# Performance work log

Measured on AMD Instinct MI355X. Metric: run time of the kernel, lower is better.

Reference implementation:

```python
import jax, jax.numpy as jnp
import numpy as np
import math

EMSIZE = 512
NX = 2048        # emsize * (layer_id+1), layer_id=3
H = NX // EMSIZE # 4 heads of size EMSIZE (grow_head path)
B, S = 4, 2048
EPS = 1e-5


def _layernorm(x, g, b):
    u = jnp.mean(x, axis=-1, keepdims=True)
    s = jnp.mean((x - u) ** 2, axis=-1, keepdims=True)
    return g * (x - u) / jnp.sqrt(s + EPS) + b


def _gelu(x):
    # OpenAI tanh-approx gelu, exactly as in source
    return 0.5 * x * (1.0 + jnp.tanh(jnp.sqrt(2.0 / jnp.pi) * (x + 0.044715 * x ** 3)))


def setup_inputs() -> dict:
    key = jax.random.key(0)
    ks = jax.random.split(key, 8)
    std = 0.02
    return {
        "x": jax.random.normal(ks[0], (B, S, NX), jnp.float32),
        "w_qkv": jax.random.normal(ks[1], (NX, 3 * NX), jnp.float32) * std,
        "b_qkv": jnp.zeros((3 * NX,), jnp.float32),
        "w_ao": jax.random.normal(ks[2], (NX, NX), jnp.float32) * std,
        "b_ao": jnp.zeros((NX,), jnp.float32),
        "ln1_g": jnp.ones((NX,), jnp.float32),
        "ln1_b": jnp.zeros((NX,), jnp.float32),
        "w_fc": jax.random.normal(ks[3], (NX, 4 * NX), jnp.float32) * std,
        "b_fc": jnp.zeros((4 * NX,), jnp.float32),
        "w_pr": jax.random.normal(ks[4], (4 * NX, NX), jnp.float32) * std,
        "b_pr": jnp.zeros((NX,), jnp.float32),
        "ln2_g": jnp.ones((NX,), jnp.float32),
        "ln2_b": jnp.zeros((NX,), jnp.float32),
        "w_out": jax.random.normal(ks[5], (NX, EMSIZE), jnp.float32) * std,
        "b_out": jnp.zeros((EMSIZE,), jnp.float32),
    }


def reference(x, w_qkv, b_qkv, w_ao, b_ao, ln1_g, ln1_b, w_fc, b_fc,
              w_pr, b_pr, ln2_g, ln2_b, w_out, b_out):
    Bx, Sx, _ = x.shape
    # --- multi-head attention ---
    qkv = x @ w_qkv + b_qkv                       # [B,S,3*NX]
    q, k, v = jnp.split(qkv, 3, axis=-1)
    q = q.reshape(Bx, Sx, H, EMSIZE).transpose(0, 2, 1, 3)  # [B,H,S,E]
    k = k.reshape(Bx, Sx, H, EMSIZE).transpose(0, 2, 1, 3)
    v = v.reshape(Bx, Sx, H, EMSIZE).transpose(0, 2, 1, 3)
    w = jnp.einsum("bhqe,bhke->bhqk", q, k) / jnp.sqrt(jnp.float32(EMSIZE))
    alen = jnp.arange(Sx)
    mask = alen[None, :] <= alen[:, None]          # causal [S,S]
    # source: w*mask + -1e9*(1-mask) == where(mask, w, -1e9)
    w = jnp.where(mask[None, None], w, jnp.float32(-1e9))
    w = jax.nn.softmax(w, axis=-1)
    a = jnp.einsum("bhqk,bhke->bhqe", w, v)        # [B,H,S,E]
    a = a.transpose(0, 2, 1, 3).reshape(Bx, Sx, NX)
    a = a @ w_ao + b_ao
    # --- residual + LN + MLP + LN ---
    n = _layernorm(x + a, ln1_g, ln1_b)
    m = (_gelu(n @ w_fc + b_fc)) @ w_pr + b_pr
    h = _layernorm(n + m, ln2_g, ln2_b)
    # --- final projection + grow_head concat ---
    h = h @ w_out + b_out                          # [B,S,EMSIZE]
    h = h.reshape(Bx, Sx, 1, EMSIZE)
    j = x.reshape(Bx, Sx, H, EMSIZE)
    out = jnp.concatenate([j, h], axis=-2)         # [B,S,H+1,E]
    return out.reshape(Bx, Sx, (H + 1) * EMSIZE)
```

## Files before the change

### kernel.cpp

```cpp
#include <hip/hip_runtime.h>
#include <hip/hip_bf16.h>
#include <math.h>

using bf16 = __hip_bfloat16;
typedef __attribute__((ext_vector_type(8))) short s16x8;
typedef __attribute__((ext_vector_type(4))) float f32x4;

struct __align__(16) B8 { bf16 v[8]; };
struct __align__(8)  B4 { bf16 v[4]; };

__device__ __forceinline__ float b2f(bf16 x){ return __bfloat162float(x); }
__device__ __forceinline__ bf16  f2b(float x){ return __float2bfloat16(x); }

enum { EPI_QKV=0, EPI_AO=3, EPI_FC=4, EPI_PR=5, EPI_OUT=6 };

#define SCHED0 __builtin_amdgcn_sched_barrier(0)
#define PRIO1  __builtin_amdgcn_s_setprio(1)
#define PRIO0  __builtin_amdgcn_s_setprio(0)
#define BAR    __builtin_amdgcn_s_barrier()
#define VM8    asm volatile("s_waitcnt vmcnt(8)" ::: "memory")
#define VM4    asm volatile("s_waitcnt vmcnt(4)" ::: "memory")
#define VM2    asm volatile("s_waitcnt vmcnt(2)" ::: "memory")
#define VM0    asm volatile("s_waitcnt vmcnt(0)" ::: "memory")
#define LGKM0  asm volatile("s_waitcnt lgkmcnt(0)" ::: "memory")
#define AS1    const __attribute__((address_space(1))) void*
#define AS3    __attribute__((address_space(3))) void*

template<int EPI>
__launch_bounds__(512, 2)
__global__ void gemm256(const bf16* __restrict__ A, const bf16* __restrict__ B,
                        void* __restrict__ Cv, const float* __restrict__ bias,
                        const void* __restrict__ res,
                        int K, int lda, int ldb, int ldc, int ldres, int nbx)
{
    extern __shared__ __align__(16) bf16 lds[];
    bf16* Asl = lds;
    bf16* Bsl = lds + 32768;

    const int nwg = (int)gridDim.x;
    int wg = (int)blockIdx.x;
    if ((nwg & 7) == 0) wg = (wg & 7)*(nwg >> 3) + (wg >> 3);
    const int bx = wg % nbx, by = wg / nbx;
    const long m0 = (long)by*256, n0 = (long)bx*256;

    const int tid = threadIdx.x, wave = tid>>6, lane = tid&63;
    const int wr = wave>>2, wc = wave&3;
    const int NT = K>>6;

    const int fr = lane&15;
    const int fc = (lane>>4) ^ ((fr>>1)&3);
    const bf16* aRd = Asl + (wr*128 + fr)*32 + fc*8;
    const bf16* bRd = Bsl + (wc*64  + fr)*32 + fc*8;

    #define LDA4(dst, slot, mq) { \
        dst[0] = *(const s16x8*)(aRd + (slot)*8192 + (mq)*2048);        \
        dst[1] = *(const s16x8*)(aRd + (slot)*8192 + (mq)*2048 + 512);  \
        dst[2] = *(const s16x8*)(aRd + (slot)*8192 + (mq)*2048 + 1024); \
        dst[3] = *(const s16x8*)(aRd + (slot)*8192 + (mq)*2048 + 1536); }
    #define LDB4(dst, slot) { \
        dst[0] = *(const s16x8*)(bRd + (slot)*8192);        \
        dst[1] = *(const s16x8*)(bRd + (slot)*8192 + 512);  \
        dst[2] = *(const s16x8*)(bRd + (slot)*8192 + 1024); \
        dst[3] = *(const s16x8*)(bRd + (slot)*8192 + 1536); }

    const int grow = tid>>2;
    const int gch  = (tid&3) ^ ((grow>>1)&3);
    const bf16* aP0 = A + (m0 + grow)*(long)lda + gch*8;
    const bf16* aP1 = aP0 + 128*(long)lda;
    const bf16* bP0 = B + (n0 + grow)*(long)ldb + gch*8;
    const bf16* bP1 = bP0 + 128*(long)ldb;
    bf16* aWr = Asl + wave*512;
    bf16* bWr = Bsl + wave*512;

    #define STGA(slot, koff) { \
        __builtin_amdgcn_global_load_lds((AS1)(aP0 + (koff)), (AS3)(aWr + (slot)*8192), 16, 0, 0); \
        __builtin_amdgcn_global_load_lds((AS1)(aP1 + (koff)), (AS3)(aWr + (slot)*8192 + 4096), 16, 0, 0); }
    #define STGB(slot, koff) { \
        __builtin_amdgcn_global_load_lds((AS1)(bP0 + (koff)), (AS3)(bWr + (slot)*8192), 16, 0, 0); \
        __builtin_amdgcn_global_load_lds((AS1)(bP1 + (koff)), (AS3)(bWr + (slot)*8192 + 4096), 16, 0, 0); }

    f32x4 acc[8][4];
    #pragma unroll
    for (int i=0;i<8;++i)
        #pragma unroll
        for (int j=0;j<4;++j)
            #pragma unroll
            for (int r=0;r<4;++r) acc[i][j][r] = 0.f;

    auto CL = [&](int mq, const s16x8* af, const s16x8* bf){
        #pragma unroll
        for (int ii=0; ii<4; ++ii)
            #pragma unroll
            for (int j=0; j<4; ++j)
                acc[mq*4+ii][j] = __builtin_amdgcn_mfma_f32_16x16x32_bf16(af[ii], bf[j], acc[mq*4+ii][j], 0,0,0);
    };

    s16x8 af0[4], af1[4], bf0[4], bf1[4];

    STGA(0,0);  STGB(0,0);
    STGA(1,32); STGB(1,32);
    STGA(2,64); STGB(2,64);
    VM8; SCHED0; BAR;
    LDB4(bf0, 0); LDA4(af0, 0, 0);
    STGA(3,96);
    SCHED0; BAR;

    for (int TT=0; TT<=NT-4; TT+=2){
        PRIO1; CL(0,af0,bf0); PRIO0;
        LDA4(af1, 0, 1);
        STGB(3, 96);
        VM8; SCHED0; BAR;
        PRIO1; CL(1,af1,bf0); PRIO0;
        LDB4(bf1, 1); LDA4(af0, 1, 0);
        STGA(0, 128);
        SCHED0; BAR;
        PRIO1; CL(0,af0,bf1); PRIO0;
        LDA4(af1, 1, 1);
        STGB(0, 128);
        VM8; SCHED0; BAR;
        PRIO1; CL(1,af1,bf1); PRIO0;
        LDB4(bf0, 2); LDA4(af0, 2, 0);
        STGA(1, 160);
        SCHED0; BAR;
        PRIO1; CL(0,af0,bf0); PRIO0;
        LDA4(af1, 2, 1);
        STGB(1, 160);
        VM8; SCHED0; BAR;
        PRIO1; CL(1,af1,bf0); PRIO0;
        LDB4(bf1, 3); LDA4(af0, 3, 0);
        STGA(2, 192);
        SCHED0; BAR;
        PRIO1; CL(0,af0,bf1); PRIO0;
        LDA4(af1, 3, 1);
        STGB(2, 192);
        VM8; SCHED0; BAR;
        PRIO1; CL(1,af1,bf1); PRIO0;
        LDB4(bf0, 0); LDA4(af0, 0, 0);
        STGA(3, 224);
        SCHED0; BAR;
        aP0 += 128; aP1 += 128; bP0 += 128; bP1 += 128;
    }

    PRIO1; CL(0,af0,bf0); PRIO0;
    LDA4(af1, 0, 1);
    STGB(3, 96);
    VM8; SCHED0; BAR;
    PRIO1; CL(1,af1,bf0); PRIO0;
    LDB4(bf1, 1); LDA4(af0, 1, 0);
    SCHED0; BAR;
    PRIO1; CL(0,af0,bf1); PRIO0;
    LDA4(af1, 1, 1);
    VM4; SCHED0; BAR;
    PRIO1; CL(1,af1,bf1); PRIO0;
    LDB4(bf0, 2); LDA4(af0, 2, 0);
    SCHED0; BAR;
    PRIO1; CL(0,af0,bf0); PRIO0;
    LDA4(af1, 2, 1);
    VM0; SCHED0; BAR;
    PRIO1; CL(1,af1,bf0); PRIO0;
    LDB4(bf1, 3); LDA4(af0, 3, 0);
    SCHED0; BAR;
    PRIO1; CL(0,af0,bf1); PRIO0;
    LDA4(af1, 3, 1);
    PRIO1; CL(1,af1,bf1); PRIO0;

    #undef STGA
    #undef STGB
    #undef LDA4
    #undef LDB4

    const int colB = lane&15;
    const int row4 = (lane>>4)*4;
    #pragma unroll
    for (int i=0;i<8;++i){
        #pragma unroll
        for (int j=0;j<4;++j){
            const long mmb = m0 + wr*128 + i*16 + row4;
            const long nn  = n0 + wc*64  + j*16 + colB;
            #pragma unroll
            for (int r=0;r<4;++r){
                const long mm = mmb + r;
                const float v = acc[i][j][r];
                if constexpr (EPI==EPI_AO){
                    ((float*)Cv)[mm*ldc + nn] = v + bias[nn] + ((const float*)res)[mm*ldres + nn];
                } else if constexpr (EPI==EPI_PR){
                    ((float*)Cv)[mm*ldc + nn] = v + bias[nn] + b2f(((const bf16*)res)[mm*ldres + nn]);
                } else if constexpr (EPI==EPI_FC){
                    const float tt = v + bias[nn];
                    const float g = 0.5f*tt*(1.f + tanhf(0.7978845608028654f*(tt + 0.044715f*tt*tt*tt)));
                    ((bf16*)Cv)[mm*ldc + nn] = f2b(g);
                } else if constexpr (EPI==EPI_OUT){
                    ((float*)Cv)[mm*ldc + nn] = v + bias[nn];
                } else {
                    ((bf16*)Cv)[mm*ldc + nn] = f2b(v + bias[nn]);
                }
            }
        }
    }
}

__launch_bounds__(512, 2)
__global__ void fattn(const bf16* __restrict__ qkv, const bf16* __restrict__ vt,
                      bf16* __restrict__ outp)
{
    extern __shared__ __align__(16) bf16 sh[];
    bf16* sQ = sh;
    bf16* sK = sh + 32768;
    bf16* sP = sh + 57344;
    bf16* sV = sh + 65536;
    float* part = (float*)(sh + 32768);

    const int bid = blockIdx.x;
    const int xcd = bid&7, t5 = bid>>3, rnd = t5>>5, ci = t5&31;
    const int bh = xcd*2 + rnd, b = bh>>2, h = bh&3;
    const int ib = 31 - ci;
    const int njb = (ib>>1) + 1;
    const int tid = threadIdx.x, wave = tid>>6, lane = tid&63;
    const int wr = wave>>2, wc = wave&3;
    const int fr = lane&15, fg = lane>>4;

    const bf16* Qg = qkv + ((long)b*2048 + ib*64)*6144 + h*512;
    const bf16* Kg = qkv + (long)b*2048*6144 + 2048 + h*512;
    const bf16* Vtb = vt + (long)bh*1048576;
    const float SCALE = 0.044194173824159216f;

    #define STGQ { _Pragma("unroll") for (int l=0;l<8;++l){                          \
        const int row = l*8 + (tid>>6);                                              \
        const int c   = (tid&63) ^ (row&7);                                          \
        __builtin_amdgcn_global_load_lds((AS1)(Qg + (long)row*6144 + c*8),           \
            (AS3)(sQ + l*4096 + wave*512 + lane*8), 16,0,0); } }
    #define STGK(slot, ec, KJ) { _Pragma("unroll") for (int l=0;l<2;++l){            \
        const int row = l*64 + (tid>>3);                                             \
        const int c   = (tid&7) ^ (row&7);                                           \
        __builtin_amdgcn_global_load_lds((AS1)((KJ) + (long)row*6144 + (ec)*64 + c*8),\
            (AS3)(sK + (slot)*8192 + l*4096 + wave*512 + lane*8), 16,0,0); } }
    #define STGV(buf, kf, eh, VJ) { _Pragma("unroll") for (int l=0;l<2;++l){         \
        const int row = l*128 + (tid>>2);                                            \
        const int c   = (tid&3) ^ ((row + (row>>2))&3);                              \
        __builtin_amdgcn_global_load_lds((AS1)((VJ) + (long)((eh)*256+row)*2048 + (kf)*32 + c*8),\
            (AS3)(sV + (buf)*8192 + l*4096 + wave*512 + lane*8), 16,0,0); } }

    f32x4 acc[2][8];
    #pragma unroll
    for (int m=0;m<2;++m)
        #pragma unroll
        for (int j=0;j<8;++j)
            #pragma unroll
            for (int r=0;r<4;++r) acc[m][j][r] = 0.f;
    float l_l[2][4];
    #pragma unroll
    for (int m=0;m<2;++m){ l_l[m][0]=0.f; l_l[m][1]=0.f; l_l[m][2]=0.f; l_l[m][3]=0.f; }

    const bf16* KgJ = Kg;
    const bf16* VtJ = Vtb;

    STGQ;
    STGK(0, 0, KgJ);
    STGK(1, 1, KgJ);
    VM2; SCHED0; BAR;

    for (int jb=0; jb<njb; ++jb){
        const bool last = (jb == njb-1);
        f32x4 sacc[2][2];
        #pragma unroll
        for (int m=0;m<2;++m)
            #pragma unroll
            for (int nf=0;nf<2;++nf)
                #pragma unroll
                for (int r=0;r<4;++r) sacc[m][nf][r] = 0.f;

        #pragma unroll
        for (int ec=0; ec<8; ++ec){
            const int slot = ec%3;
            s16x8 qa[2][2], kb[2][2];
            #pragma unroll
            for (int m=0;m<2;++m)
                #pragma unroll
                for (int kk=0;kk<2;++kk){
                    const int row = wr*32 + m*16 + fr;
                    const int c = (ec*2+kk)*4 + fg;
                    qa[m][kk] = *(const s16x8*)(sQ + row*512 + ((c ^ (row&7))*8));
                }
            #pragma unroll
            for (int nf=0;nf<2;++nf)
                #pragma unroll
                for (int kk=0;kk<2;++kk){
                    const int row = wc*32 + nf*16 + fr;
                    const int c = kk*4 + fg;
                    kb[nf][kk] = *(const s16x8*)(sK + slot*8192 + row*64 + ((c ^ (row&7))*8));
                }
            if (ec < 6) STGK((ec+2)%3, ec+2, KgJ);
            PRIO1;
            #pragma unroll
            for (int m=0;m<2;++m)
                #pragma unroll
                for (int nf=0;nf<2;++nf)
                    #pragma unroll
                    for (int kk=0;kk<2;++kk)
                        sacc[m][nf] = __builtin_amdgcn_mfma_f32_16x16x32_bf16(qa[m][kk], kb[nf][kk], sacc[m][nf], 0,0,0);
            PRIO0;
            if (ec < 6) { VM2; } else if (ec == 6) { VM0; }
            SCHED0; BAR;
        }

        const int doff = (njb-1)*128 - ib*64;
        #pragma unroll
        for (int m=0;m<2;++m)
            #pragma unroll
            for (int nf=0;nf<2;++nf)
                #pragma unroll
                for (int r=0;r<4;++r){
                    float pv = __expf(sacc[m][nf][r]*SCALE - 4.0f);
                    const int rl = wr*32 + m*16 + fg*4 + r;
                    const int cl = wc*32 + nf*16 + fr;
                    if (last && (cl + doff > rl)) pv = 0.f;
                    sP[rl*128 + (((cl>>3) ^ (rl&15))*8) + (cl&7)] = f2b(pv);
                    l_l[m][r] += pv;
                }
        STGV(0, 0, 0, VtJ);
        if (!last){ STGK(0, 0, KgJ + 786432); STGK(1, 1, KgJ + 786432); }
        if (!last){ VM4; } else { VM0; }
        LGKM0; SCHED0; BAR;

        s16x8 pa[2];
        #pragma unroll
        for (int v=0; v<8; ++v){
            const int kf = v>>1, eh = v&1, buf = v&1;
            if (eh == 0){
                #pragma unroll
                for (int m=0;m<2;++m){
                    const int row = wr*32 + m*16 + fr;
                    const int c = kf*4 + fg;
                    pa[m] = *(const s16x8*)(sP + row*128 + ((c ^ (row&15))*8));
                }
            }
            s16x8 vb[4];
            #pragma unroll
            for (int nf=0;nf<4;++nf){
                const int row = wc*64 + nf*16 + fr;
                vb[nf] = *(const s16x8*)(sV + buf*8192 + row*32 + (((fg ^ ((row + (row>>2))&3)))*8));
            }
            if (v < 7) STGV((v+1)&1, (v+1)>>1, (v+1)&1, VtJ);
            PRIO1;
            #pragma unroll
            for (int m=0;m<2;++m)
                #pragma unroll
                for (int nf=0;nf<4;++nf)
                    acc[m][eh*4+nf] = __builtin_amdgcn_mfma_f32_16x16x32_bf16(pa[m], vb[nf], acc[m][eh*4+nf], 0,0,0);
            PRIO0;
            if (v < 7) { VM0; }
            SCHED0; BAR;
        }
        KgJ += 786432;
        VtJ += 128;
    }

    #pragma unroll
    for (int m=0;m<2;++m)
        #pragma unroll
        for (int r=0;r<4;++r){
            float v = l_l[m][r];
            v += __shfl_xor(v, 1); v += __shfl_xor(v, 2);
            v += __shfl_xor(v, 4); v += __shfl_xor(v, 8);
            l_l[m][r] = v;
        }
    if (fr == 0){
        #pragma unroll
        for (int m=0;m<2;++m)
            #pragma unroll
            for (int r=0;r<4;++r)
                part[(wr*32 + m*16 + fg*4 + r)*4 + wc] = l_l[m][r];
    }
    LGKM0; SCHED0; BAR;

    bf16* orow = outp + ((long)b*2048 + ib*64)*2048 + h*512;
    #pragma unroll
    for (int m=0;m<2;++m)
        #pragma unroll
        for (int r=0;r<4;++r){
            const int rl = wr*32 + m*16 + fg*4 + r;
            const f32x4 pp = *(const f32x4*)(part + rl*4);
            const float rinv = 1.f/(pp[0]+pp[1]+pp[2]+pp[3]);
            #pragma unroll
            for (int j=0;j<8;++j){
                const int e = (j>>2)*256 + wc*64 + (j&3)*16 + fr;
                orow[(long)rl*2048 + e] = f2b(acc[m][j][r]*rinv);
            }
        }
    #undef STGQ
    #undef STGK
    #undef STGV
}

__launch_bounds__(256)
__global__ void wtrans(const float* __restrict__ W, bf16* __restrict__ Wt, int Kd, int Nd){
    __shared__ float t[32][33];
    const int n0 = blockIdx.x*32, k0 = blockIdx.y*32;
    const int tx = threadIdx.x&31, ty = threadIdx.x>>5;
    #pragma unroll
    for (int i=0;i<32;i+=8) t[ty+i][tx] = W[(long)(k0+ty+i)*Nd + n0+tx];
    __syncthreads();
    #pragma unroll
    for (int i=0;i<32;i+=8) Wt[(long)(n0+ty+i)*Kd + k0+tx] = f2b(t[tx][ty+i]);
}

__launch_bounds__(256)
__global__ void vtrans(const bf16* __restrict__ qkv, bf16* __restrict__ vt){
    const int z = blockIdx.z, b = z>>2, h = z&3;
    const bf16* in = qkv + (long)b*12582912 + 4096 + h*512;
    bf16* outp = vt + (long)z*1048576;
    __shared__ bf16 t[32][33];
    const int e0 = blockIdx.x*32, s0 = blockIdx.y*32;
    const int tx = threadIdx.x&31, ty = threadIdx.x>>5;
    #pragma unroll
    for (int i=0;i<32;i+=8) t[ty+i][tx] = in[(long)(s0+ty+i)*6144 + e0+tx];
    __syncthreads();
    #pragma unroll
    for (int i=0;i<32;i+=8) outp[(long)(e0+ty+i)*2048 + s0+tx] = t[tx][ty+i];
}

__launch_bounds__(256)
__global__ void cvt_f32_bf16(const float* __restrict__ in, bf16* __restrict__ outp){
    const long i = ((long)blockIdx.x*256 + threadIdx.x)*4;
    const float4 v = *(const float4*)&in[i];
    B4 o; o.v[0]=f2b(v.x); o.v[1]=f2b(v.y); o.v[2]=f2b(v.z); o.v[3]=f2b(v.w);
    *reinterpret_cast<B4*>(&outp[i]) = o;
}

__launch_bounds__(256)
__global__ void jcopy(const float* __restrict__ x, float* __restrict__ outp){
    const long idx = ((long)blockIdx.x*256 + threadIdx.x)*4;
    const long r = idx>>11, c = idx&2047;
    *(float4*)&outp[r*2560 + c] = *(const float4*)&x[idx];
}

__launch_bounds__(256)
__global__ void ln_rows(const float* __restrict__ in, const float* __restrict__ gw,
                        const float* __restrict__ bw, bf16* __restrict__ outp){
    const long r = blockIdx.x;
    const float* row = in + r*2048;
    const int tid = threadIdx.x, k0 = tid*8;
    const float4 a = *(const float4*)&row[k0];
    const float4 c = *(const float4*)&row[k0+4];
    float v[8] = {a.x,a.y,a.z,a.w,c.x,c.y,c.z,c.w};
    float s = 0.f, qq = 0.f;
    #pragma unroll
    for (int i=0;i<8;++i){ s += v[i]; qq += v[i]*v[i]; }
    #pragma unroll
    for (int o=32;o;o>>=1){ s += __shfl_xor(s,o); qq += __shfl_xor(qq,o); }
    __shared__ float s1[4], s2[4];
    if ((tid&63)==0){ s1[tid>>6]=s; s2[tid>>6]=qq; }
    __syncthreads();
    s  = s1[0]+s1[1]+s1[2]+s1[3];
    qq = s2[0]+s2[1]+s2[2]+s2[3];
    const float mean = s*(1.f/2048.f);
    const float var  = qq*(1.f/2048.f) - mean*mean;
    const float inv  = rsqrtf(var + 1e-5f);
    const float4 g1 = *(const float4*)&gw[k0];
    const float4 g2 = *(const float4*)&gw[k0+4];
    const float4 b1 = *(const float4*)&bw[k0];
    const float4 b2 = *(const float4*)&bw[k0+4];
    const float gg[8] = {g1.x,g1.y,g1.z,g1.w,g2.x,g2.y,g2.z,g2.w};
    const float bb[8] = {b1.x,b1.y,b1.z,b1.w,b2.x,b2.y,b2.z,b2.w};
    B8 o;
    #pragma unroll
    for (int i=0;i<8;++i) o.v[i] = f2b((v[i]-mean)*inv*gg[i] + bb[i]);
    *reinterpret_cast<B8*>(&outp[r*2048 + k0]) = o;
}

extern "C" void kernel_launch(void* const* d_in, const int* in_sizes, int n_in,
                              void* d_out, int out_size, void* d_ws, size_t ws_size,
                              hipStream_t stream)
{
    (void)in_sizes; (void)n_in; (void)out_size;
    const float* x     = (const float*)d_in[0];
    const float* w_qkv = (const float*)d_in[1];
    const float* b_qkv = (const float*)d_in[2];
    const float* w_ao  = (const float*)d_in[3];
    const float* b_ao  = (const float*)d_in[4];
    const float* ln1g  = (const float*)d_in[5];
    const float* ln1b  = (const float*)d_in[6];
    const float* w_fc  = (const float*)d_in[7];
    const float* b_fc  = (const float*)d_in[8];
    const float* w_pr  = (const float*)d_in[9];
    const float* b_pr  = (const float*)d_in[10];
    const float* ln2g  = (const float*)d_in[11];
    const float* ln2b  = (const float*)d_in[12];
    const float* w_out = (const float*)d_in[13];
    const float* b_out = (const float*)d_in[14];
    float* out = (float*)d_out;
    char* ws = (char*)d_ws;

    const size_t NEEDED = 245366784ull;
    if (ws_size < NEEDED) return;

    bf16*  xb     = (bf16*)(ws);
    bf16*  qkv    = (bf16*)(ws + 33554432ull);
    float* r1     = (float*)(ws + 33554432ull);
    bf16*  fcact  = (bf16*)(ws);
    bf16*  vt     = (bf16*)(ws + 134217728ull);
    bf16*  Wfc_t  = (bf16*)(ws + 134217728ull);
    float* rbufc  = (float*)(ws + 134217728ull);
    bf16*  Wpr_t  = (bf16*)(ws + 167772160ull);
    bf16*  Wqkv_t = (bf16*)(ws + 201326592ull);
    bf16*  nbuf   = (bf16*)(ws + 201326592ull);
    bf16*  Wao_t  = (bf16*)(ws + 234881024ull);
    bf16*  Wout_t = (bf16*)(ws + 243269632ull);

    const dim3 T(256);
    const int SMEM = 131072;
    const int SMEM_A = 163840;
    hipFuncSetAttribute((const void*)gemm256<EPI_QKV>, hipFuncAttributeMaxDynamicSharedMemorySize, SMEM);
    hipFuncSetAttribute((const void*)gemm256<EPI_AO>,  hipFuncAttributeMaxDynamicSharedMemorySize, SMEM);
    hipFuncSetAttribute((const void*)gemm256<EPI_FC>,  hipFuncAttributeMaxDynamicSharedMemorySize, SMEM);
    hipFuncSetAttribute((const void*)gemm256<EPI_PR>,  hipFuncAttributeMaxDynamicSharedMemorySize, SMEM);
    hipFuncSetAttribute((const void*)gemm256<EPI_OUT>, hipFuncAttributeMaxDynamicSharedMemorySize, SMEM);
    hipFuncSetAttribute((const void*)fattn,            hipFuncAttributeMaxDynamicSharedMemorySize, SMEM_A);

    wtrans<<<dim3(192,64),T,0,stream>>>(w_qkv, Wqkv_t, 2048, 6144);
    wtrans<<<dim3(64,64), T,0,stream>>>(w_ao,  Wao_t,  2048, 2048);
    wtrans<<<dim3(16,64), T,0,stream>>>(w_out, Wout_t, 2048, 512);
    cvt_f32_bf16<<<16384,T,0,stream>>>(x, xb);

    gemm256<EPI_QKV><<<dim3(768),dim3(512),SMEM,stream>>>(xb, Wqkv_t, qkv, b_qkv, nullptr,
        2048, 2048, 2048, 6144, 0, 24);
    vtrans<<<dim3(16,64,16),T,0,stream>>>(qkv, vt);

    fattn<<<dim3(512),dim3(512),SMEM_A,stream>>>(qkv, vt, xb);

    gemm256<EPI_AO><<<dim3(256),dim3(512),SMEM,stream>>>(xb, Wao_t, r1, b_ao, x,
        2048, 2048, 2048, 2048, 2048, 8);
    ln_rows<<<8192,T,0,stream>>>(r1, ln1g, ln1b, nbuf);

    wtrans<<<dim3(256,64),T,0,stream>>>(w_fc, Wfc_t, 2048, 8192);
    wtrans<<<dim3(64,256),T,0,stream>>>(w_pr, Wpr_t, 8192, 2048);
    gemm256<EPI_FC><<<dim3(1024),dim3(512),SMEM,stream>>>(nbuf, Wfc_t, fcact, b_fc, nullptr,
        2048, 2048, 2048, 8192, 0, 32);
    for (int c=0; c<2; ++c){
        const long ro = (long)c*4096;
        gemm256<EPI_PR><<<dim3(128),dim3(512),SMEM,stream>>>(
            fcact + ro*8192, Wpr_t, rbufc, b_pr, nbuf + ro*2048,
            8192, 8192, 8192, 2048, 2048, 8);
        ln_rows<<<4096,T,0,stream>>>(rbufc, ln2g, ln2b, nbuf + ro*2048);
    }

    gemm256<EPI_OUT><<<dim3(64),dim3(512),SMEM,stream>>>(nbuf, Wout_t, out + 2048, b_out, nullptr,
        2048, 2048, 2048, 2560, 0, 2);
    jcopy<<<16384,T,0,stream>>>(x, out);
}
```

Before: 1.215 ms.

## Restructure GEMM main loop to BK=64 quadrant schedule and merge PR GEMM launches

```diff
diff --git a/kernel.cpp b/kernel.cpp
--- a/kernel.cpp
+++ b/kernel.cpp
@@ -12,13 +12,13 @@
 __device__ __forceinline__ float b2f(bf16 x){ return __bfloat162float(x); }
 __device__ __forceinline__ bf16  f2b(float x){ return __float2bfloat16(x); }
 
-enum { EPI_QKV=0, EPI_AO=3, EPI_FC=4, EPI_PR=5, EPI_OUT=6 };
+enum { EPI_QKV=0, EPI_AO=3, EPI_FC=4, EPI_PRB=5, EPI_OUT=6 };
 
 #define SCHED0 __builtin_amdgcn_sched_barrier(0)
 #define PRIO1  __builtin_amdgcn_s_setprio(1)
 #define PRIO0  __builtin_amdgcn_s_setprio(0)
 #define BAR    __builtin_amdgcn_s_barrier()
-#define VM8    asm volatile("s_waitcnt vmcnt(8)" ::: "memory")
+#define VM6    asm volatile("s_waitcnt vmcnt(6)" ::: "memory")
 #define VM4    asm volatile("s_waitcnt vmcnt(4)" ::: "memory")
 #define VM2    asm volatile("s_waitcnt vmcnt(2)" ::: "memory")
 #define VM0    asm volatile("s_waitcnt vmcnt(0)" ::: "memory")
@@ -46,157 +46,128 @@
     const int tid = threadIdx.x, wave = tid>>6, lane = tid&63;
     const int wr = wave>>2, wc = wave&3;
     const int NT = K>>6;
-
-    const int fr = lane&15;
-    const int fc = (lane>>4) ^ ((fr>>1)&3);
-    const bf16* aRd = Asl + (wr*128 + fr)*32 + fc*8;
-    const bf16* bRd = Bsl + (wc*64  + fr)*32 + fc*8;
-
-    #define LDA4(dst, slot, mq) { \
-        dst[0] = *(const s16x8*)(aRd + (slot)*8192 + (mq)*2048);        \
-        dst[1] = *(const s16x8*)(aRd + (slot)*8192 + (mq)*2048 + 512);  \
-        dst[2] = *(const s16x8*)(aRd + (slot)*8192 + (mq)*2048 + 1024); \
-        dst[3] = *(const s16x8*)(aRd + (slot)*8192 + (mq)*2048 + 1536); }
-    #define LDB4(dst, slot) { \
-        dst[0] = *(const s16x8*)(bRd + (slot)*8192);        \
-        dst[1] = *(const s16x8*)(bRd + (slot)*8192 + 512);  \
-        dst[2] = *(const s16x8*)(bRd + (slot)*8192 + 1024); \
-        dst[3] = *(const s16x8*)(bRd + (slot)*8192 + 1536); }
-
-    const int grow = tid>>2;
-    const int gch  = (tid&3) ^ ((grow>>1)&3);
-    const bf16* aP0 = A + (m0 + grow)*(long)lda + gch*8;
-    const bf16* aP1 = aP0 + 128*(long)lda;
-    const bf16* bP0 = B + (n0 + grow)*(long)ldb + gch*8;
-    const bf16* bP1 = bP0 + 128*(long)ldb;
-    bf16* aWr = Asl + wave*512;
-    bf16* bWr = Bsl + wave*512;
-
-    #define STGA(slot, koff) { \
-        __builtin_amdgcn_global_load_lds((AS1)(aP0 + (koff)), (AS3)(aWr + (slot)*8192), 16, 0, 0); \
-        __builtin_amdgcn_global_load_lds((AS1)(aP1 + (koff)), (AS3)(aWr + (slot)*8192 + 4096), 16, 0, 0); }
-    #define STGB(slot, koff) { \
-        __builtin_amdgcn_global_load_lds((AS1)(bP0 + (koff)), (AS3)(bWr + (slot)*8192), 16, 0, 0); \
-        __builtin_amdgcn_global_load_lds((AS1)(bP1 + (koff)), (AS3)(bWr + (slot)*8192 + 4096), 16, 0, 0); }
-
-    f32x4 acc[8][4];
-    #pragma unroll
-    for (int i=0;i<8;++i)
-        #pragma unroll
-        for (int j=0;j<4;++j)
-            #pragma unroll
-            for (int r=0;r<4;++r) acc[i][j][r] = 0.f;
-
-    auto CL = [&](int mq, const s16x8* af, const s16x8* bf){
-        #pragma unroll
-        for (int ii=0; ii<4; ++ii)
-            #pragma unroll
-            for (int j=0; j<4; ++j)
-                acc[mq*4+ii][j] = __builtin_amdgcn_mfma_f32_16x16x32_bf16(af[ii], bf[j], acc[mq*4+ii][j], 0,0,0);
-    };
-
-    s16x8 af0[4], af1[4], bf0[4], bf1[4];
-
-    STGA(0,0);  STGB(0,0);
-    STGA(1,32); STGB(1,32);
-    STGA(2,64); STGB(2,64);
-    VM8; SCHED0; BAR;
-    LDB4(bf0, 0); LDA4(af0, 0, 0);
-    STGA(3,96);
-    SCHED0; BAR;
-
-    for (int TT=0; TT<=NT-4; TT+=2){
-        PRIO1; CL(0,af0,bf0); PRIO0;
-        LDA4(af1, 0, 1);
-        STGB(3, 96);
-        VM8; SCHED0; BAR;
-        PRIO1; CL(1,af1,bf0); PRIO0;
-        LDB4(bf1, 1); LDA4(af0, 1, 0);
-        STGA(0, 128);
-        SCHED0; BAR;
-        PRIO1; CL(0,af0,bf1); PRIO0;
-        LDA4(af1, 1, 1);
-        STGB(0, 128);
-        VM8; SCHED0; BAR;
-        PRIO1; CL(1,af1,bf1); PRIO0;
-        LDB4(bf0, 2); LDA4(af0, 2, 0);
-        STGA(1, 160);
-        SCHED0; BAR;
-        PRIO1; CL(0,af0,bf0); PRIO0;
-        LDA4(af1, 2, 1);
-        STGB(1, 160);
-        VM8; SCHED0; BAR;
-        PRIO1; CL(1,af1,bf0); PRIO0;
-        LDB4(bf1, 3); LDA4(af0, 3, 0);
-        STGA(2, 192);
-        SCHED0; BAR;
-        PRIO1; CL(0,af0,bf1); PRIO0;
-        LDA4(af1, 3, 1);
-        STGB(2, 192);
-        VM8; SCHED0; BAR;
-        PRIO1; CL(1,af1,bf1); PRIO0;
-        LDB4(bf0, 0); LDA4(af0, 0, 0);
-        STGA(3, 224);
-        SCHED0; BAR;
-        aP0 += 128; aP1 += 128; bP0 += 128; bP1 += 128;
+    const int fr = lane&15, fg = lane>>4;
+
+    const int ck0 = fg ^ (fr&7);
+    const int ck1 = (4+fg) ^ (fr&7);
+    const bf16* aRd0 = Asl + wr*4096 + fr*64 + ck0*8;
+    const bf16* aRd1 = Asl + wr*4096 + fr*64 + ck1*8;
+    const bf16* bRd0 = Bsl + wc*2048 + fr*64 + ck0*8;
+    const bf16* bRd1 = Bsl + wc*2048 + fr*64 + ck1*8;
+
+    #define RDA(d, rh) { _Pragma("unroll") for (int i=0;i<4;++i){ \
+        a[i][0] = *(const s16x8*)(aRd0 + (d)*16384 + (rh)*8192 + i*1024); \
+        a[i][1] = *(const s16x8*)(aRd1 + (d)*16384 + (rh)*8192 + i*1024); } }
+    #define RDB(dst, d, ch) { _Pragma("unroll") for (int j=0;j<2;++j){ \
+        dst[j][0] = *(const s16x8*)(bRd0 + (d)*16384 + (ch)*8192 + j*1024); \
+        dst[j][1] = *(const s16x8*)(bRd1 + (d)*16384 + (ch)*8192 + j*1024); } }
+
+    const int grow = tid>>3;
+    const int gc0  = (tid&7) ^ (grow&7);
+    const bf16* aP = A + (m0 + grow)*(long)lda + gc0*8;
+    const bf16* bP = B + (n0 + grow)*(long)ldb + gc0*8;
+
+    #define STGA(sd, sh, koff) { _Pragma("unroll") for (int l=0;l<2;++l) \
+        __builtin_amdgcn_global_load_lds((AS1)(aP + ((sh)*128 + l*64)*(long)lda + (koff)), \
+            (AS3)(Asl + (sd)*16384 + (sh)*8192 + l*4096 + wave*512 + lane*8), 16, 0, 0); }
+    #define STGB(sd, sh, koff) { _Pragma("unroll") for (int l=0;l<2;++l) \
+        __builtin_amdgcn_global_load_lds((AS1)(bP + ((sh)*128 + l*64)*(long)ldb + (koff)), \
+            (AS3)(Bsl + (sd)*16384 + (sh)*8192 + l*4096 + wave*512 + lane*8), 16, 0, 0); }
+
+    f32x4 acc[2][4][2][2];
+    #pragma unroll
+    for (int rh=0;rh<2;++rh)
+        #pragma unroll
+        for (int i=0;i<4;++i)
+            #pragma unroll
+            for (int ch=0;ch<2;++ch)
+                #pragma unroll
+                for (int j=0;j<2;++j)
+                    #pragma unroll
+                    for (int r=0;r<4;++r) acc[rh][i][ch][j][r] = 0.f;
+
+    #define MM(rh, ch, BB) { PRIO1; \
+        _Pragma("unroll") for (int i=0;i<4;++i) \
+        _Pragma("unroll") for (int j=0;j<2;++j) \
+        _Pragma("unroll") for (int kk=0;kk<2;++kk) \
+            acc[rh][i][ch][j] = __builtin_amdgcn_mfma_f32_16x16x32_bf16(a[i][kk], BB[j][kk], acc[rh][i][ch][j], 0,0,0); \
+        PRIO0; }
+
+    s16x8 a[4][2], b0[2][2], b1[2][2];
+
+    STGA(0,0,0);  STGB(0,1,0);  STGA(0,1,0);  STGB(0,0,0);
+    STGA(1,0,64); STGB(1,1,64); STGA(1,1,64);
+    VM6; SCHED0; BAR;
+
+    for (int t=0; t<=NT-4; t+=2){
+        RDB(b0,0,0); RDA(0,0); STGB(1,0,64);
+        SCHED0; BAR; LGKM0; MM(0,0,b0); SCHED0; BAR;
+        RDB(b1,0,1);           STGA(0,0,128);
+        SCHED0; BAR; LGKM0; MM(0,1,b1); SCHED0; BAR;
+        RDA(0,1);              STGB(0,1,128);
+        SCHED0; BAR; LGKM0; MM(1,1,b1); SCHED0; BAR;
+                               STGA(0,1,128); VM6;
+        SCHED0; BAR; LGKM0; MM(1,0,b0); SCHED0; BAR;
+        RDB(b0,1,0); RDA(1,0); STGB(0,0,128);
+        SCHED0; BAR; LGKM0; MM(0,0,b0); SCHED0; BAR;
+        RDB(b1,1,1);           STGA(1,0,192);
+        SCHED0; BAR; LGKM0; MM(0,1,b1); SCHED0; BAR;
+        RDA(1,1);              STGB(1,1,192);
+        SCHED0; BAR; LGKM0; MM(1,1,b1); SCHED0; BAR;
+                               STGA(1,1,192); VM6;
+        SCHED0; BAR; LGKM0; MM(1,0,b0); SCHED0; BAR;
+        aP += 128; bP += 128;
     }
 
-    PRIO1; CL(0,af0,bf0); PRIO0;
-    LDA4(af1, 0, 1);
-    STGB(3, 96);
-    VM8; SCHED0; BAR;
-    PRIO1; CL(1,af1,bf0); PRIO0;
-    LDB4(bf1, 1); LDA4(af0, 1, 0);
-    SCHED0; BAR;
-    PRIO1; CL(0,af0,bf1); PRIO0;
-    LDA4(af1, 1, 1);
-    VM4; SCHED0; BAR;
-    PRIO1; CL(1,af1,bf1); PRIO0;
-    LDB4(bf0, 2); LDA4(af0, 2, 0);
-    SCHED0; BAR;
-    PRIO1; CL(0,af0,bf0); PRIO0;
-    LDA4(af1, 2, 1);
-    VM0; SCHED0; BAR;
-    PRIO1; CL(1,af1,bf0); PRIO0;
-    LDB4(bf1, 3); LDA4(af0, 3, 0);
-    SCHED0; BAR;
-    PRIO1; CL(0,af0,bf1); PRIO0;
-    LDA4(af1, 3, 1);
-    PRIO1; CL(1,af1,bf1); PRIO0;
-
+    RDB(b0,0,0); RDA(0,0); STGB(1,0,64);
+    SCHED0; BAR; LGKM0; MM(0,0,b0); SCHED0; BAR;
+    RDB(b1,0,1);
+    SCHED0; BAR; LGKM0; MM(0,1,b1); SCHED0; BAR;
+    RDA(0,1);
+    SCHED0; BAR; LGKM0; MM(1,1,b1); SCHED0; BAR;
+    VM0;
+    SCHED0; BAR; LGKM0; MM(1,0,b0); SCHED0; BAR;
+    RDB(b0,1,0); RDA(1,0);
+    SCHED0; BAR; LGKM0; MM(0,0,b0); SCHED0; BAR;
+    RDB(b1,1,1);
+    SCHED0; BAR; LGKM0; MM(0,1,b1); SCHED0; BAR;
+    RDA(1,1);
+    SCHED0; BAR; LGKM0; MM(1,1,b1); SCHED0; BAR;
+    MM(1,0,b0);
+
+    #undef RDA
+    #undef RDB
     #undef STGA
     #undef STGB
-    #undef LDA4
-    #undef LDB4
-
-    const int colB = lane&15;
-    const int row4 = (lane>>4)*4;
-    #pragma unroll
-    for (int i=0;i<8;++i){
-        #pragma unroll
-        for (int j=0;j<4;++j){
-            const long mmb = m0 + wr*128 + i*16 + row4;
-            const long nn  = n0 + wc*64  + j*16 + colB;
-            #pragma unroll
-            for (int r=0;r<4;++r){
-                const long mm = mmb + r;
-                const float v = acc[i][j][r];
-                if constexpr (EPI==EPI_AO){
-                    ((float*)Cv)[mm*ldc + nn] = v + bias[nn] + ((const float*)res)[mm*ldres + nn];
-                } else if constexpr (EPI==EPI_PR){
-                    ((float*)Cv)[mm*ldc + nn] = v + bias[nn] + b2f(((const bf16*)res)[mm*ldres + nn]);
-                } else if constexpr (EPI==EPI_FC){
-                    const float tt = v + bias[nn];
-                    const float g = 0.5f*tt*(1.f + tanhf(0.7978845608028654f*(tt + 0.044715f*tt*tt*tt)));
-                    ((bf16*)Cv)[mm*ldc + nn] = f2b(g);
-                } else if constexpr (EPI==EPI_OUT){
-                    ((float*)Cv)[mm*ldc + nn] = v + bias[nn];
-                } else {
-                    ((bf16*)Cv)[mm*ldc + nn] = f2b(v + bias[nn]);
-                }
-            }
-        }
-    }
+    #undef MM
+
+    #pragma unroll
+    for (int rh=0;rh<2;++rh)
+        #pragma unroll
+        for (int i=0;i<4;++i)
+            #pragma unroll
+            for (int ch=0;ch<2;++ch)
+                #pragma unroll
+                for (int j=0;j<2;++j)
+                    #pragma unroll
+                    for (int r=0;r<4;++r){
+                        const long mm = m0 + rh*128 + wr*64 + i*16 + fg*4 + r;
+                        const long nn = n0 + ch*128 + wc*32 + j*16 + fr;
+                        const float v = acc[rh][i][ch][j][r];
+                        if constexpr (EPI==EPI_AO){
+                            ((float*)Cv)[mm*ldc + nn] = v + bias[nn] + ((const float*)res)[mm*ldres + nn];
+                        } else if constexpr (EPI==EPI_PRB){
+                            ((bf16*)Cv)[mm*ldc + nn] = f2b(v + bias[nn] + b2f(((const bf16*)res)[mm*ldres + nn]));
+                        } else if constexpr (EPI==EPI_FC){
+                            const float tt = v + bias[nn];
+                            const float g = 0.5f*tt*(1.f + tanhf(0.7978845608028654f*(tt + 0.044715f*tt*tt*tt)));
+                            ((bf16*)Cv)[mm*ldc + nn] = f2b(g);
+                        } else if constexpr (EPI==EPI_OUT){
+                            ((float*)Cv)[mm*ldc + nn] = v + bias[nn];
+                        } else {
+                            ((bf16*)Cv)[mm*ldc + nn] = f2b(v + bias[nn]);
+                        }
+                    }
 }
 
 __launch_bounds__(512, 2)
@@ -434,15 +405,24 @@
     *(float4*)&outp[r*2560 + c] = *(const float4*)&x[idx];
 }
 
+template<int BF>
 __launch_bounds__(256)
-__global__ void ln_rows(const float* __restrict__ in, const float* __restrict__ gw,
+__global__ void ln_rows(const void* __restrict__ inp, const float* __restrict__ gw,
                         const float* __restrict__ bw, bf16* __restrict__ outp){
     const long r = blockIdx.x;
-    const float* row = in + r*2048;
     const int tid = threadIdx.x, k0 = tid*8;
-    const float4 a = *(const float4*)&row[k0];
-    const float4 c = *(const float4*)&row[k0+4];
-    float v[8] = {a.x,a.y,a.z,a.w,c.x,c.y,c.z,c.w};
+    float v[8];
+    if constexpr (BF){
+        const bf16* row = (const bf16*)inp + r*2048;
+        const B8 x = *reinterpret_cast<const B8*>(&row[k0]);
+        #pragma unroll
+        for (int i=0;i<8;++i) v[i] = b2f(x.v[i]);
+    } else {
+        const float* row = (const float*)inp + r*2048;
+        const float4 a = *(const float4*)&row[k0];
+        const float4 c = *(const float4*)&row[k0+4];
+        v[0]=a.x; v[1]=a.y; v[2]=a.z; v[3]=a.w; v[4]=c.x; v[5]=c.y; v[6]=c.z; v[7]=c.w;
+    }
     float s = 0.f, qq = 0.f;
     #pragma unroll
     for (int i=0;i<8;++i){ s += v[i]; qq += v[i]*v[i]; }
@@ -455,7 +435,7 @@
     qq = s2[0]+s2[1]+s2[2]+s2[3];
     const float mean = s*(1.f/2048.f);
     const float var  = qq*(1.f/2048.f) - mean*mean;
-    const float inv  = rsqrtf(var + 1e-5f);
+    const float rinv = rsqrtf(var + 1e-5f);
     const float4 g1 = *(const float4*)&gw[k0];
     const float4 g2 = *(const float4*)&gw[k0+4];
     const float4 b1 = *(const float4*)&bw[k0];
@@ -464,7 +444,7 @@
     const float bb[8] = {b1.x,b1.y,b1.z,b1.w,b2.x,b2.y,b2.z,b2.w};
     B8 o;
     #pragma unroll
-    for (int i=0;i<8;++i) o.v[i] = f2b((v[i]-mean)*inv*gg[i] + bb[i]);
+    for (int i=0;i<8;++i) o.v[i] = f2b((v[i]-mean)*rinv*gg[i] + bb[i]);
     *reinterpret_cast<B8*>(&outp[r*2048 + k0]) = o;
 }
 
@@ -500,7 +480,7 @@
     bf16*  fcact  = (bf16*)(ws);
     bf16*  vt     = (bf16*)(ws + 134217728ull);
     bf16*  Wfc_t  = (bf16*)(ws + 134217728ull);
-    float* rbufc  = (float*)(ws + 134217728ull);
+    bf16*  rbufB  = (bf16*)(ws + 134217728ull);
     bf16*  Wpr_t  = (bf16*)(ws + 167772160ull);
     bf16*  Wqkv_t = (bf16*)(ws + 201326592ull);
     bf16*  nbuf   = (bf16*)(ws + 201326592ull);
@@ -510,12 +490,12 @@
     const dim3 T(256);
     const int SMEM = 131072;
     const int SMEM_A = 163840;
-    hipFuncSetAttribute((const void*)gemm256<EPI_QKV>, hipFuncAttributeMaxDynamicSharedMemorySize, SMEM);
-    hipFuncSetAttribute((const void*)gemm256<EPI_AO>,  hipFuncAttributeMaxDynamicSharedMemorySize, SMEM);
-    hipFuncSetAttribute((const void*)gemm256<EPI_FC>,  hipFuncAttributeMaxDynamicSharedMemorySize, SMEM);
-    hipFuncSetAttribute((const void*)gemm256<EPI_PR>,  hipFuncAttributeMaxDynamicSharedMemorySize, SMEM);
-    hipFuncSetAttribute((const void*)gemm256<EPI_OUT>, hipFuncAttributeMaxDynamicSharedMemorySize, SMEM);
-    hipFuncSetAttribute((const void*)fattn,            hipFuncAttributeMaxDynamicSharedMemorySize, SMEM_A);
+    (void)hipFuncSetAttribute((const void*)gemm256<EPI_QKV>, hipFuncAttributeMaxDynamicSharedMemorySize, SMEM);
+    (void)hipFuncSetAttribute((const void*)gemm256<EPI_AO>,  hipFuncAttributeMaxDynamicSharedMemorySize, SMEM);
+    (void)hipFuncSetAttribute((const void*)gemm256<EPI_FC>,  hipFuncAttributeMaxDynamicSharedMemorySize, SMEM);
+    (void)hipFuncSetAttribute((const void*)gemm256<EPI_PRB>, hipFuncAttributeMaxDynamicSharedMemorySize, SMEM);
+    (void)hipFuncSetAttribute((const void*)gemm256<EPI_OUT>, hipFuncAttributeMaxDynamicSharedMemorySize, SMEM);
+    (void)hipFuncSetAttribute((const void*)fattn,            hipFuncAttributeMaxDynamicSharedMemorySize, SMEM_A);
 
     wtrans<<<dim3(192,64),T,0,stream>>>(w_qkv, Wqkv_t, 2048, 6144);
     wtrans<<<dim3(64,64), T,0,stream>>>(w_ao,  Wao_t,  2048, 2048);
@@ -530,19 +510,15 @@
 
     gemm256<EPI_AO><<<dim3(256),dim3(512),SMEM,stream>>>(xb, Wao_t, r1, b_ao, x,
         2048, 2048, 2048, 2048, 2048, 8);
-    ln_rows<<<8192,T,0,stream>>>(r1, ln1g, ln1b, nbuf);
+    ln_rows<0><<<8192,T,0,stream>>>(r1, ln1g, ln1b, nbuf);
 
     wtrans<<<dim3(256,64),T,0,stream>>>(w_fc, Wfc_t, 2048, 8192);
     wtrans<<<dim3(64,256),T,0,stream>>>(w_pr, Wpr_t, 8192, 2048);
     gemm256<EPI_FC><<<dim3(1024),dim3(512),SMEM,stream>>>(nbuf, Wfc_t, fcact, b_fc, nullptr,
         2048, 2048, 2048, 8192, 0, 32);
-    for (int c=0; c<2; ++c){
-        const long ro = (long)c*4096;
-        gemm256<EPI_PR><<<dim3(128),dim3(512),SMEM,stream>>>(
-            fcact + ro*8192, Wpr_t, rbufc, b_pr, nbuf + ro*2048,
-            8192, 8192, 8192, 2048, 2048, 8);
-        ln_rows<<<4096,T,0,stream>>>(rbufc, ln2g, ln2b, nbuf + ro*2048);
-    }
+    gemm256<EPI_PRB><<<dim3(256),dim3(512),SMEM,stream>>>(fcact, Wpr_t, rbufB, b_pr, nbuf,
+        8192, 8192, 8192, 2048, 2048, 8);
+    ln_rows<1><<<8192,T,0,stream>>>(rbufB, ln2g, ln2b, nbuf);
 
     gemm256<EPI_OUT><<<dim3(64),dim3(512),SMEM,stream>>>(nbuf, Wout_t, out + 2048, b_out, nullptr,
         2048, 2048, 2048, 2560, 0, 2);
```

Measured after the change: 1.080 ms. 11.1% less time.
